# Optimization experiments

Hardware: AMD Instinct MI355X
Metric: run time of the kernel (lower is better)

## Reference

```python
import jax, jax.numpy as jnp
import numpy as np

H, O, M, D, B = 4, 32, 128, 16, 1024
JITTER = 1e-4


def k_rbf(theta, X, Y):
    # theta: [H, 1+D] (log sf2, log lengthscales); X: [O,Mx,D]; Y: [O,My,D]
    sf2 = jnp.exp(theta[:, 0])[:, None, None, None]          # [H,1,1,1]
    ls = jnp.exp(theta[:, 1:])                               # [H,D]
    Xs = X[None] / ls[:, None, None, :]                      # [H,O,Mx,D]
    Ys = Y[None] / ls[:, None, None, :]                      # [H,O,My,D]
    d2 = ((Xs ** 2).sum(-1)[..., :, None]
          + (Ys ** 2).sum(-1)[..., None, :]
          - 2.0 * jnp.einsum('homd,hond->homn', Xs, Ys))
    return sf2 * jnp.exp(-0.5 * jnp.maximum(d2, 0.0))


def vec2tril(vec, m):
    r, c = jnp.tril_indices(m)
    L = jnp.zeros(vec.shape[:-1] + (m, m), vec.dtype)
    return L.at[..., r, c].set(vec)


def _st(Lmat, rhs):
    return jax.scipy.linalg.solve_triangular(Lmat, rhs, lower=True)


def setup_inputs() -> dict:
    key = jax.random.key(0)
    ks = jax.random.split(key, 8)
    eye = jnp.eye(M, dtype=jnp.float32)
    return {
        'x': jax.random.normal(ks[0], (B, D), jnp.float32),
        'z': 0.5 * jax.random.normal(ks[1], (O, M, D), jnp.float32),
        'u_mean': 0.5 * jax.random.normal(ks[2], (O, M, 1), jnp.float32),
        'u_tril_vec': 0.1 * jax.random.normal(ks[3], (O, M * (M + 1) // 2), jnp.float32),
        'm_old': 0.5 * jax.random.normal(ks[4], (O, M, 1), jnp.float32),
        'L_old': jnp.tril(0.1 * jax.random.normal(ks[5], (O, M, M), jnp.float32)) + eye,
        'z_old': 0.5 * jax.random.normal(ks[6], (O, M, D), jnp.float32),
        'theta': 0.1 * jax.random.normal(ks[7], (H, D + 1), jnp.float32),
    }


def reference(x, z, u_mean, u_tril_vec, m_old, L_old, z_old, theta):
    dt = x.dtype
    u_tril = vec2tril(u_tril_vec, M)                          # [O,M,M]
    eyeM = jnp.eye(M, dtype=dt)

    # ---- linear_gauss_joint (one previous task) ----
    kuf = k_rbf(theta, z_old, z)                              # [H,O,M,M]
    kuu = k_rbf(theta, z_old, z_old)                          # [H,O,M,M]
    Lkuu = jnp.linalg.cholesky(kuu + JITTER * eyeM)
    LKinvKuf = _st(Lkuu, kuf)
    m_oldh = jnp.broadcast_to(m_old[None], (H, O, M, 1))
    L_oldh = jnp.broadcast_to(L_old[None], (H, O, M, M))
    LKinvm = _st(Lkuu, m_oldh)
    Am = jnp.einsum('...ij,...ik->...jk', LKinvKuf, LKinvm)   # A @ m_old, [H,O,M,1]
    m_new = Am + u_mean[None]
    m_joint = jnp.concatenate([m_oldh, m_new], axis=-2)       # [H,O,2M,1]

    S_old = jnp.einsum('...ji,...ki->...jk', L_oldh, L_oldh)
    LKinvLS = _st(Lkuu, L_oldh)
    AtX = jnp.einsum('...ij,...ik->...jk', LKinvLS, LKinvKuf)  # [H,O,M,M]
    SoldAt = jnp.einsum('...ji,...ik->...jk', L_oldh, AtX)
    ASoldt = jnp.swapaxes(SoldAt, -1, -2)
    S_cur = jnp.einsum('...ji,...ki->...jk', u_tril, u_tril)[None]
    ASoldAt = jnp.einsum('...ij,...ik->...jk', AtX, AtX)
    cov_joint = jnp.concatenate([
        jnp.concatenate([S_old, SoldAt], axis=-1),
        jnp.concatenate([ASoldt, S_cur + ASoldAt], axis=-1)], axis=-2)
    eye2M = jnp.eye(2 * M, dtype=dt)
    L_joint = jnp.linalg.cholesky(cov_joint + JITTER * eye2M)  # [H,O,2M,2M]
    z_joint = jnp.concatenate([z_old, z], axis=-2)             # [O,2M,D]

    # ---- linear_gauss_conditional_diag ----
    xb = jnp.broadcast_to(x[None], (O, B, D))
    kuf2 = k_rbf(theta, z_joint, xb)                           # [H,O,2M,B]
    kuu2 = k_rbf(theta, z_joint, z_joint)
    Lk2 = jnp.linalg.cholesky(kuu2 + JITTER * eye2M)
    LKinvu = _st(Lk2, m_joint)
    LKinvKuf2 = _st(Lk2, kuf2)
    kff_diag = jnp.exp(theta[:, 0])[:, None, None]             # [H,1,1]
    diag1 = (LKinvKuf2 ** 2).sum(axis=-2)                      # [H,O,B]
    LKinvLs = _st(Lk2, L_joint)
    vec2 = jnp.einsum('...ij,...ik->...jk', LKinvLs, LKinvKuf2)
    diag2 = (vec2 ** 2).sum(axis=-2)
    mu = jnp.einsum('...ij,...ik->...jk', LKinvKuf2, LKinvu)[..., 0]
    var = kff_diag - diag1 + diag2
    return mu, var
```

## Files before the change

kernel.cpp:

```cpp
#include <hip/hip_runtime.h>

#define H_ 4
#define O_ 32
#define HO 128
#define M_ 128
#define M2 256
#define D_ 16
#define B_ 1024
#define JIT 1e-4f

typedef unsigned short ushort_t;
typedef __bf16 v8bf __attribute__((ext_vector_type(8)));
typedef float v16f __attribute__((ext_vector_type(16)));
typedef unsigned short v8us __attribute__((ext_vector_type(8)));
typedef unsigned short v4us __attribute__((ext_vector_type(4)));

__device__ inline void splitbf(float v, ushort_t& hb, ushort_t& lb) {
    unsigned int u = __float_as_uint(v);
    hb = (ushort_t)(u >> 16);
    float hf = __uint_as_float((unsigned int)hb << 16);
    float r = v - hf;
    lb = (ushort_t)(__float_as_uint(r) >> 16);
}
__device__ inline float bf2f(ushort_t u) { return __uint_as_float((unsigned int)u << 16); }

__device__ __forceinline__ float rdlane(float v, int l) {
    return __int_as_float(__builtin_amdgcn_readlane(__float_as_int(v), l));
}

__global__ __launch_bounds__(256) void k_prekuu2(const float* __restrict__ theta,
                                                 const float* __restrict__ x,
                                                 const float* __restrict__ z,
                                                 const float* __restrict__ z_old,
                                                 float* __restrict__ SF2,
                                                 float* __restrict__ XS, float* __restrict__ XN,
                                                 float* __restrict__ ZS, float* __restrict__ ZN,
                                                 float* __restrict__ K2) {
    int bb = blockIdx.x, t = threadIdx.x;
    __shared__ float zs[M2][D_];
    __shared__ float zn[M2];
    __shared__ float ls[D_];
    if (bb == 144) {
        if (t < H_) SF2[t] = __expf(theta[t * (D_ + 1)]);
        return;
    }
    if (bb >= 128) {
        int j = (bb - 128) * 256 + t;
        int h = j >> 10, b = j & 1023;
        if (t < D_) ls[t] = __expf(-theta[h * (D_ + 1) + 1 + t]);
        __syncthreads();
        float s = 0.f;
#pragma unroll
        for (int d = 0; d < D_; d++) {
            float v = x[b * D_ + d] * ls[d];
            XS[(long)j * D_ + d] = v;
            s += v * v;
        }
        XN[j] = s;
        return;
    }
    int pair = bb, h = pair >> 5, o = pair & 31, i = t;
    if (t < D_) ls[t] = __expf(-theta[h * (D_ + 1) + 1 + t]);
    __syncthreads();
    const float* src = (i < M_) ? (z_old + ((long)o * M_ + i) * D_)
                                : (z + ((long)o * M_ + (i - M_)) * D_);
    float s = 0.f;
#pragma unroll
    for (int d = 0; d < D_; d++) {
        float v = src[d] * ls[d];
        zs[i][d] = v;
        ZS[((long)pair * M2 + i) * D_ + d] = v;
        s += v * v;
    }
    zn[i] = s;
    ZN[pair * M2 + i] = s;
    __syncthreads();
    float sf2 = __expf(theta[h * (D_ + 1)]);
    float my[D_];
#pragma unroll
    for (int d = 0; d < D_; d++) my[d] = zs[i][d];
    float myn = zn[i];
    for (int q = 0; q < M2; q++) {
        float dot = 0.f;
#pragma unroll
        for (int d = 0; d < D_; d++) dot += zs[q][d] * my[d];
        float d2 = fmaxf(zn[q] + myn - 2.f * dot, 0.f);
        float v = sf2 * __expf(-0.5f * d2);
        if (q == i) v += JIT;
        K2[(long)pair * M2 * M2 + (long)q * M2 + i] = v;
    }
}

__device__ __forceinline__ void choltri_body(const float* __restrict__ S, int ldsrc,
                                             float* __restrict__ Li, long b1, int t,
                                             float* __restrict__ Ap, float* __restrict__ Lv,
                                             float* __restrict__ Ws4, float* __restrict__ Tm,
                                             float* __restrict__ rdia) {
    for (int e = t; e < M_ * (M_ + 1) / 2; e += 256) {
        int i = (int)((sqrtf(8.f * e + 1.f) - 1.f) * 0.5f);
        while ((i + 1) * (i + 2) / 2 <= e) i++;
        while (i * (i + 1) / 2 > e) i--;
        int j = e - i * (i + 1) / 2;
        Ap[e] = S[(long)i * ldsrc + j];
    }
    __syncthreads();

    int lane = t & 63;
    int wav = t >> 6;
    int r = lane & 31;

    for (int kb = 0; kb < 4; kb++) {
        int c0 = kb * 32;
        if (wav == 0) {
            float a[32];
            int gr = c0 + r;
            int base = gr * (gr + 1) / 2 + c0;
#pragma unroll
            for (int j = 0; j < 32; j++) a[j] = Ap[base + j];
#pragma unroll
            for (int k = 0; k < 32; k++) {
                float dk = rdlane(a[k], k);
                float rs = rsqrtf(dk);
                rs = rs * (1.5f - 0.5f * dk * rs * rs);
                a[k] *= rs;
                if (lane == k) rdia[c0 + k] = rs;
#pragma unroll
                for (int j = k + 1; j < 32; j++) {
                    float ljk = rdlane(a[k], j);
                    a[j] = fmaf(-a[k], ljk, a[j]);
                }
            }
            if (lane < 32) {
#pragma unroll
                for (int j = 0; j < 32; j++)
                    if (j <= r) Ap[base + j] = a[j];
            }
        }
        __syncthreads();
        int R = 96 - c0;
        if (R > 0) {
            if (t < R) {
                int gi = c0 + 32 + t;
                int pb = gi * (gi + 1) / 2 + c0;
                float xr[32];
#pragma unroll
                for (int j = 0; j < 32; j++) xr[j] = Ap[pb + j];
#pragma unroll
                for (int q = 0; q < 32; q++) {
                    float xq = xr[q] * rdia[c0 + q];
                    xr[q] = xq;
#pragma unroll
                    for (int j = q + 1; j < 32; j++)
                        xr[j] = fmaf(-xq, Ap[(c0 + j) * (c0 + j + 1) / 2 + c0 + q], xr[j]);
                }
#pragma unroll
                for (int j = 0; j < 32; j++) Ap[pb + j] = xr[j];
            }
            __syncthreads();
            int nb = R >> 2;
            int ntile = nb * (nb + 1) / 2;
            for (int tp = t; tp < ntile; tp += 256) {
                int bi = (int)((sqrtf(8.f * tp + 1.f) - 1.f) * 0.5f);
                while ((bi + 1) * (bi + 2) / 2 <= tp) bi++;
                while (bi * (bi + 1) / 2 > tp) bi--;
                int bj = tp - bi * (bi + 1) / 2;
                int i0 = c0 + 32 + bi * 4, j0 = c0 + 32 + bj * 4;
                float acc[4][4] = {};
                for (int k = 0; k < 32; k++) {
                    float av[4], bv[4];
#pragma unroll
                    for (int q = 0; q < 4; q++) av[q] = Ap[(i0 + q) * (i0 + q + 1) / 2 + c0 + k];
#pragma unroll
                    for (int rr = 0; rr < 4; rr++) bv[rr] = Ap[(j0 + rr) * (j0 + rr + 1) / 2 + c0 + k];
#pragma unroll
                    for (int q = 0; q < 4; q++)
#pragma unroll
                        for (int rr = 0; rr < 4; rr++) acc[q][rr] += av[q] * bv[rr];
                }
#pragma unroll
                for (int q = 0; q < 4; q++)
#pragma unroll
                    for (int rr = 0; rr < 4; rr++) {
                        int gi = i0 + q, gj = j0 + rr;
                        if (gj <= gi) Ap[gi * (gi + 1) / 2 + gj] -= acc[q][rr];
                    }
            }
            __syncthreads();
        }
    }

    {
        int pb = wav;
        int c0 = pb * 32;
        float a[32];
        int gr = c0 + r;
        int base = gr * (gr + 1) / 2 + c0;
#pragma unroll
        for (int j = 0; j < 32; j++) a[j] = Ap[base + j];
        float wr[32];
#pragma unroll
        for (int i = 0; i < 32; i++) {
            float rdi = rdia[c0 + i];
            float acc = 0.f;
#pragma unroll
            for (int j = 0; j < i; j++) {
                float lij = rdlane(a[j], i);
                acc = fmaf(lij, wr[j], acc);
            }
            wr[i] = (i == r) ? rdi : -acc * rdi;
        }
        if (lane < 32) {
            float* Wp = Ws4 + pb * 1056;
#pragma unroll
            for (int i = 0; i < 32; i++) Wp[i * 33 + r] = wr[i];
        }
    }
    __syncthreads();

    for (int e = t; e < 16384; e += 256) {
        int i = e >> 7, j = e & 127;
        int bi = i >> 5, bj = j >> 5;
        float v = 0.f;
        if (bi == bj) v = Ws4[bi * 1056 + (i & 31) * 33 + (j & 31)];
        Lv[i * 132 + j] = v;
    }
    __syncthreads();
    for (int d = 1; d < 4; d++) {
        int nblk = 4 - d;
        int ne = nblk * 256;
        for (int p = t; p < ne; p += 256) {
            int b = p >> 8, rc = p & 255;
            int rr = rc >> 3, c4 = (rc & 7) * 4;
            int ib = b + d;
            int grow = ib * 32 + rr;
            int abase = grow * (grow + 1) / 2;
            float a0 = 0.f, a1 = 0.f, a2 = 0.f, a3 = 0.f;
            for (int k = b; k < ib; k++) {
                const float* Arow = Ap + abase + k * 32;
                const float* L0 = Lv + (k * 32) * 132 + b * 32 + c4;
#pragma unroll
                for (int q = 0; q < 32; q++) {
                    float av = Arow[q];
                    const float* Lr = L0 + q * 132;
                    a0 = fmaf(av, Lr[0], a0);
                    a1 = fmaf(av, Lr[1], a1);
                    a2 = fmaf(av, Lr[2], a2);
                    a3 = fmaf(av, Lr[3], a3);
                }
            }
            float* Tp = Tm + b * 1152 + rr * 36 + c4;
            Tp[0] = a0; Tp[1] = a1; Tp[2] = a2; Tp[3] = a3;
        }
        __syncthreads();
        for (int p = t; p < ne; p += 256) {
            int b = p >> 8, rc = p & 255;
            int rr = rc >> 3, c4 = (rc & 7) * 4;
            int ib = b + d;
            const float* Wp = Ws4 + ib * 1056 + rr * 33;
            const float* T0 = Tm + b * 1152 + c4;
            float a0 = 0.f, a1 = 0.f, a2 = 0.f, a3 = 0.f;
#pragma unroll
            for (int q = 0; q < 32; q++) {
                float wq = Wp[q];
                const float* Tq = T0 + q * 36;
                a0 = fmaf(wq, Tq[0], a0);
                a1 = fmaf(wq, Tq[1], a1);
                a2 = fmaf(wq, Tq[2], a2);
                a3 = fmaf(wq, Tq[3], a3);
            }
            float* Op = Lv + (ib * 32 + rr) * 132 + b * 32 + c4;
            Op[0] = -a0; Op[1] = -a1; Op[2] = -a2; Op[3] = -a3;
        }
        __syncthreads();
    }
    for (int e = t; e < 16384; e += 256) {
        int i = e >> 7, j = e & 127;
        Li[b1 + e] = Lv[i * 132 + j];
    }
}

#define SH_TOTAL (8256 + 16896 + 4224 + 3456 + 128)

__global__ __launch_bounds__(256) void k_choltri_tl(const float* __restrict__ src,
                                                    float* __restrict__ Li,
                                                    const float* __restrict__ L_old,
                                                    const float* __restrict__ vec,
                                                    ushort_t* __restrict__ WTh,
                                                    ushort_t* __restrict__ WTl) {
    int bb = blockIdx.x, t = threadIdx.x;
    __shared__ __align__(16) float SH[SH_TOTAL];
    if (bb < 128) {
        choltri_body(src + (long)bb * ((long)M2 * M2), M2, Li, (long)bb * 16384, t,
                     SH, SH + 8256, SH + 8256 + 16896, SH + 8256 + 16896 + 4224,
                     SH + 8256 + 16896 + 4224 + 3456);
        return;
    }
    int pair = bb - 128, o = pair & 31;
    long b2 = (long)pair * 65536;
    float* vs = SH;
    float(*tile)[33] = (float(*)[33])(SH + 8256);
    for (int e = t; e < M_ * (M_ + 1) / 2; e += 256) vs[e] = vec[(long)o * (M_ * (M_ + 1) / 2) + e];
    __syncthreads();
    for (int e = t; e < 16384; e += 256) {
        int n = e >> 7, k = e & 127;
        float v = (k >= n) ? vs[k * (k + 1) / 2 + n] : 0.f;
        ushort_t hb, lb;
        splitbf(v, hb, lb);
        long a = b2 + (long)(128 + n) * 256 + 128 + k;
        WTh[a] = hb;
        WTl[a] = lb;
    }
    for (int e = t; e < 16384; e += 256) {
        int n = e >> 7, k = e & 127;
        long a = b2 + (long)(128 + n) * 256 + k;
        WTh[a] = 0;
        WTl[a] = 0;
    }
    const float* sp = L_old + (long)o * 16384;
    int tx = t & 31, ty = t >> 5;
    for (int bi = 0; bi < 4; bi++)
        for (int bj = 0; bj < 4; bj++) {
            __syncthreads();
            for (int r = ty; r < 32; r += 8)
                tile[r][tx] = sp[(long)(bi * 32 + r) * 128 + bj * 32 + tx];
            __syncthreads();
            for (int r = ty; r < 32; r += 8) {
                ushort_t hb, lb;
                splitbf(tile[tx][r], hb, lb);
                long a = b2 + (long)(bj * 32 + r) * 256 + bi * 32 + tx;
                WTh[a] = hb;
                WTl[a] = lb;
            }
        }
}

__global__ __launch_bounds__(256) void k_choltri_br(const float* __restrict__ src,
                                                    float* __restrict__ Li,
                                                    const float* __restrict__ A1,
                                                    const float* __restrict__ Linv1,
                                                    float* __restrict__ T1g,
                                                    const float* __restrict__ BLW,
                                                    ushort_t* __restrict__ LTh,
                                                    ushort_t* __restrict__ LTl,
                                                    ushort_t* __restrict__ WTh,
                                                    ushort_t* __restrict__ WTl) {
    int bb = blockIdx.x, t = threadIdx.x;
    __shared__ __align__(16) float SH[SH_TOTAL];
    if (bb < 128) {
        choltri_body(src + (long)bb * ((long)M2 * M2), M2, Li, (long)bb * 16384, t,
                     SH, SH + 8256, SH + 8256 + 16896, SH + 8256 + 16896 + 4224,
                     SH + 8256 + 16896 + 4224 + 3456);
        return;
    }
    if (bb < 256) {
        int pair = bb - 128;
        long b1 = (long)pair * 16384;
        float(*As)[132] = (float(*)[132])(SH + 8256);
        float(*Bs)[132] = ((float(*)[132])(SH + 8256)) + 16;
        const float* Apt = A1 + b1;
        const float* Bpt = Linv1 + b1;
        float* Cp = T1g + (long)pair * 65536;
        int tx = t & 15, ty = t >> 4;
        float acc[8][8] = {};
        for (int kt = 0; kt < M_; kt += 16) {
#pragma unroll
            for (int q = 0; q < 8; q++) {
                int e = q * 256 + t;
                int kk = e >> 7, m = e & 127;
                As[kk][m] = Apt[(long)(kt + kk) * 128 + m];
                Bs[kk][m] = Bpt[(long)(kt + kk) * 128 + m];
            }
            __syncthreads();
#pragma unroll
            for (int kk = 0; kk < 16; kk++) {
                float a[8], b[8];
#pragma unroll
                for (int q = 0; q < 8; q++) { a[q] = As[kk][ty + 16 * q]; b[q] = Bs[kk][tx + 16 * q]; }
#pragma unroll
                for (int q = 0; q < 8; q++)
#pragma unroll
                    for (int r = 0; r < 8; r++) acc[q][r] += a[q] * b[r];
            }
            __syncthreads();
        }
#pragma unroll
        for (int q = 0; q < 8; q++)
#pragma unroll
            for (int r = 0; r < 8; r++)
                Cp[(long)(ty + 16 * q) * 128 + tx + 16 * r] = acc[q][r];
        return;
    }
    if (bb < 384) {
        int pair = bb - 256;
        long b2 = (long)pair * 65536, b1 = (long)pair * 16384;
        float(*tile)[33] = (float(*)[33])(SH + 8256);
        for (int e = t; e < 16384; e += 256) {
            int n = e >> 7, k = e & 127;
            long a = b2 + (long)(128 + n) * 256 + k;
            LTh[a] = 0;
            LTl[a] = 0;
        }
        const float* sp = Linv1 + b1;
        int tx = t & 31, ty = t >> 5;
        for (int bi = 0; bi < 4; bi++)
            for (int bj = 0; bj < 4; bj++) {
                __syncthreads();
                for (int r = ty; r < 32; r += 8)
                    tile[r][tx] = sp[(long)(bi * 32 + r) * 128 + bj * 32 + tx];
                __syncthreads();
                for (int r = ty; r < 32; r += 8) {
                    ushort_t hb, lb;
                    splitbf(tile[tx][r], hb, lb);
                    long a = b2 + (long)(bj * 32 + r) * 256 + bi * 32 + tx;
                    LTh[a] = hb;
                    LTl[a] = lb;
                }
            }
        return;
    }
    {
        int pair = bb - 384;
        long b2 = (long)pair * 65536, b1 = (long)pair * 16384;
        float(*tile)[33] = (float(*)[33])(SH + 8256);
        const float* sp = BLW + b1;
        int tx = t & 31, ty = t >> 5;
        for (int bi = 0; bi < 4; bi++)
            for (int bj = 0; bj < 4; bj++) {
                __syncthreads();
                for (int r = ty; r < 32; r += 8)
                    tile[r][tx] = sp[(long)(bi * 32 + r) * 128 + bj * 32 + tx];
                __syncthreads();
                for (int r = ty; r < 32; r += 8) {
                    ushort_t hb, lb;
                    splitbf(tile[tx][r], hb, lb);
                    long a = b2 + (long)(bj * 32 + r) * 256 + 128 + bi * 32 + tx;
                    WTh[a] = hb;
                    WTl[a] = lb;
                }
            }
    }
}

__global__ __launch_bounds__(256) void k_a1a3(const float* __restrict__ Linv1,
                                              const float* __restrict__ KUU2,
                                              const float* __restrict__ L_old,
                                              float* __restrict__ A1, float* __restrict__ A3) {
    int pair = blockIdx.x, y = blockIdx.y, o = pair & 31;
    const float* Ap = Linv1 + (long)pair * 16384;
    const float* Bp = y ? (L_old + (long)o * 16384) : (KUU2 + (long)pair * 65536 + 128);
    int ldb = y ? 128 : 256;
    float* Cp = (y ? A3 : A1) + (long)pair * 16384;
    int t = threadIdx.x, tx = t & 15, ty = t >> 4;
    __shared__ float As[16][132], Bs[16][132];
    float acc[8][8] = {};
    for (int kt = 0; kt < M_; kt += 16) {
#pragma unroll
        for (int q = 0; q < 8; q++) {
            int e = q * 256 + t;
            int m = e >> 4, kk = e & 15;
            As[kk][m] = Ap[(long)m * 128 + kt + kk];
            int kk2 = e >> 7, n = e & 127;
            Bs[kk2][n] = Bp[(long)(kt + kk2) * ldb + n];
        }
        __syncthreads();
#pragma unroll
        for (int kk = 0; kk < 16; kk++) {
            float a[8], b[8];
#pragma unroll
            for (int q = 0; q < 8; q++) { a[q] = As[kk][ty + 16 * q]; b[q] = Bs[kk][tx + 16 * q]; }
#pragma unroll
            for (int q = 0; q < 8; q++)
#pragma unroll
                for (int r = 0; r < 8; r++) acc[q][r] += a[q] * b[r];
        }
        __syncthreads();
    }
#pragma unroll
    for (int q = 0; q < 8; q++)
#pragma unroll
        for (int r = 0; r < 8; r++)
            Cp[(long)(ty + 16 * q) * 128 + tx + 16 * r] = acc[q][r];
}

__global__ __launch_bounds__(256) void k_blwschur(const float* __restrict__ A1,
                                                  const float* __restrict__ A3,
                                                  float* __restrict__ BLW,
                                                  float* __restrict__ KUU2,
                                                  const float* __restrict__ Linv1,
                                                  const float* __restrict__ m_old,
                                                  const float* __restrict__ u_mean,
                                                  float* __restrict__ MJ,
                                                  float* __restrict__ CV) {
    int pair = blockIdx.x, y = blockIdx.y, o = pair & 31;
    int t = threadIdx.x;
    if (y == 2) {
        CV[pair * 256 + t] = 0.f;
        __shared__ float mo[128], a2[128];
        if (t < 128) mo[t] = m_old[o * 128 + t];
        __syncthreads();
        if (t < 128) {
            const float* Lr = Linv1 + (long)pair * 16384 + (long)t * 128;
            float acc = 0.f;
            for (int j = 0; j <= t; j++) acc += Lr[j] * mo[j];
            a2[t] = acc;
        }
        __syncthreads();
        if (t < 128) {
            float m = 0.f;
            for (int i = 0; i < 128; i++) m += A1[(long)pair * 16384 + (long)i * 128 + t] * a2[i];
            MJ[pair * 256 + t] = mo[t];
            MJ[pair * 256 + 128 + t] = m + u_mean[o * 128 + t];
        }
        return;
    }
    const float* Ap = A1 + (long)pair * 16384;
    const float* Bp = (y ? A1 : A3) + (long)pair * 16384;
    float* Cp;
    int ldc;
    if (y) { Cp = KUU2 + (long)pair * 65536 + 128L * 256 + 128; ldc = 256; }
    else   { Cp = BLW + (long)pair * 16384; ldc = 128; }
    int tx = t & 15, ty = t >> 4;
    __shared__ float As[16][132], Bs[16][132];
    float acc[8][8] = {};
    for (int kt = 0; kt < M_; kt += 16) {
#pragma unroll
        for (int q = 0; q < 8; q++) {
            int e = q * 256 + t;
            int kk = e >> 7, m = e & 127;
            As[kk][m] = Ap[(long)(kt + kk) * 128 + m];
            Bs[kk][m] = Bp[(long)(kt + kk) * 128 + m];
        }
        __syncthreads();
#pragma unroll
        for (int kk = 0; kk < 16; kk++) {
            float a[8], b[8];
#pragma unroll
            for (int q = 0; q < 8; q++) { a[q] = As[kk][ty + 16 * q]; b[q] = Bs[kk][tx + 16 * q]; }
#pragma unroll
            for (int q = 0; q < 8; q++)
#pragma unroll
                for (int r = 0; r < 8; r++) acc[q][r] += a[q] * b[r];
        }
        __syncthreads();
    }
#pragma unroll
    for (int q = 0; q < 8; q++)
#pragma unroll
        for (int r = 0; r < 8; r++) {
            long idx = (long)(ty + 16 * q) * ldc + tx + 16 * r;
            if (y) Cp[idx] -= acc[q][r];
            else Cp[idx] = acc[q][r];
        }
}

__global__ __launch_bounds__(256) void k_blicalc2(const float* __restrict__ Linv2,
                                                  const float* __restrict__ T1g,
                                                  ushort_t* __restrict__ LTh,
                                                  ushort_t* __restrict__ LTl) {
    int pair = blockIdx.x, t = threadIdx.x, tx = t & 15, ty = t >> 4;
    long b1 = (long)pair * 16384, b2 = (long)pair * 65536;
    __shared__ float T1s[128][129];
    __shared__ float As[16][132], Bs[16][132];
    const float* Apt = Linv2 + b1;
    const float* Bpt = T1g + (long)pair * 65536;
    float acc[8][8] = {};
    for (int kt = 0; kt < M_; kt += 16) {
#pragma unroll
        for (int q = 0; q < 8; q++) {
            int e = q * 256 + t;
            int m = e >> 4, kk = e & 15;
            As[kk][m] = Apt[(long)m * 128 + kt + kk];
            int kk2 = e >> 7, n = e & 127;
            Bs[kk2][n] = Bpt[(long)(kt + kk2) * 128 + n];
        }
        __syncthreads();
#pragma unroll
        for (int kk = 0; kk < 16; kk++) {
            float a[8], b[8];
#pragma unroll
            for (int q = 0; q < 8; q++) { a[q] = As[kk][ty + 16 * q]; b[q] = Bs[kk][tx + 16 * q]; }
#pragma unroll
            for (int q = 0; q < 8; q++)
#pragma unroll
                for (int r = 0; r < 8; r++) acc[q][r] += a[q] * b[r];
        }
        __syncthreads();
    }
#pragma unroll
    for (int q = 0; q < 8; q++)
#pragma unroll
        for (int r = 0; r < 8; r++) T1s[ty + 16 * q][tx + 16 * r] = -acc[q][r];
    __syncthreads();
    for (int e = t; e < 16384; e += 256) {
        int j = e >> 7, i = e & 127;
        ushort_t hb, lb;
        splitbf(T1s[i][j], hb, lb);
        long a = b2 + (long)j * 256 + 128 + i;
        LTh[a] = hb;
        LTl[a] = lb;
    }
    __syncthreads();
    for (int e = t; e < 16384; e += 256) {
        int i = e >> 7, j = e & 127;
        T1s[i][j] = Apt[(long)i * 128 + j];
    }
    __syncthreads();
    for (int e = t; e < 16384; e += 256) {
        int n = e >> 7, k = e & 127;
        ushort_t hb, lb;
        splitbf(T1s[k][n], hb, lb);
        long a = b2 + (long)(128 + n) * 256 + 128 + k;
        LTh[a] = hb;
        LTl[a] = lb;
    }
}

#define BSTR 56
template <int TILES3>
__global__ __launch_bounds__(256) void k_bmmx(const ushort_t* __restrict__ Ah,
                                              const ushort_t* __restrict__ Al,
                                              const ushort_t* __restrict__ Bh,
                                              const ushort_t* __restrict__ Bl,
                                              float* __restrict__ Cf,
                                              ushort_t* __restrict__ Chi,
                                              ushort_t* __restrict__ Clo,
                                              const float* __restrict__ Dm,
                                              int kLoMode, float alpha,
                                              const float* __restrict__ MJv,
                                              float* __restrict__ CVat) {
    int pair = blockIdx.x;
    long base = (long)pair * 65536;
    int I0, J0, mir = 0;
    if (TILES3) {
        int qb = blockIdx.y;
        I0 = (qb == 0) ? 0 : 128;
        J0 = (qb == 2) ? 0 : I0;
        mir = (qb == 2);
    } else {
        I0 = (blockIdx.y >> 1) * 128;
        J0 = (blockIdx.y & 1) * 128;
    }
    int k0 = (kLoMode == 1) ? max(I0, J0) : (kLoMode == 2) ? J0 : 0;
    int t = threadIdx.x;
    int w = t >> 6, lane = t & 63;
    int l31 = lane & 31, lhalf = lane >> 5;
    int wy = w >> 1, wx = w & 1;

    __shared__ __align__(16) ushort_t AsH[128][BSTR], AsL[128][BSTR];
    __shared__ __align__(16) ushort_t BsH[128][BSTR], BsL[128][BSTR];

    v16f acc[2][2];
#pragma unroll
    for (int mt = 0; mt < 2; mt++)
#pragma unroll
        for (int nt = 0; nt < 2; nt++)
#pragma unroll
            for (int r = 0; r < 16; r++) acc[mt][nt][r] = 0.f;

    for (int kt = k0; kt < 256; kt += 32) {
        __syncthreads();
#pragma unroll
        for (int u = 0; u < 2; u++) {
            int idx = u * 256 + t;
            int m = idx >> 2, kc = (idx & 3) * 8;
            long arow = base + (long)(I0 + m) * 256 + kt + kc;
            long brow = base + (long)(J0 + m) * 256 + kt + kc;
            *(v8us*)&AsH[m][kc] = *(const v8us*)(Ah + arow);
            *(v8us*)&AsL[m][kc] = *(const v8us*)(Al + arow);
            *(v8us*)&BsH[m][kc] = *(const v8us*)(Bh + brow);
            *(v8us*)&BsL[m][kc] = *(const v8us*)(Bl + brow);
        }
        __syncthreads();
#pragma unroll
        for (int ks = 0; ks < 2; ks++) {
            int ko = ks * 16 + lhalf * 8;
            v8bf ah[2], al[2], bh[2], bl[2];
#pragma unroll
            for (int mt = 0; mt < 2; mt++) {
                int r = wy * 64 + mt * 32 + l31;
                ah[mt] = *(const v8bf*)&AsH[r][ko];
                al[mt] = *(const v8bf*)&AsL[r][ko];
            }
#pragma unroll
            for (int nt = 0; nt < 2; nt++) {
                int r = wx * 64 + nt * 32 + l31;
                bh[nt] = *(const v8bf*)&BsH[r][ko];
                bl[nt] = *(const v8bf*)&BsL[r][ko];
            }
#pragma unroll
            for (int mt = 0; mt < 2; mt++)
#pragma unroll
                for (int nt = 0; nt < 2; nt++) {
                    acc[mt][nt] = __builtin_amdgcn_mfma_f32_32x32x16_bf16(ah[mt], bh[nt], acc[mt][nt], 0, 0, 0);
                    acc[mt][nt] = __builtin_amdgcn_mfma_f32_32x32x16_bf16(ah[mt], bl[nt], acc[mt][nt], 0, 0, 0);
                    acc[mt][nt] = __builtin_amdgcn_mfma_f32_32x32x16_bf16(al[mt], bh[nt], acc[mt][nt], 0, 0, 0);
                }
        }
    }

    float mjc[2] = {0.f, 0.f};
    float cvmir[2] = {0.f, 0.f};
    if (MJv) {
#pragma unroll
        for (int nt = 0; nt < 2; nt++)
            mjc[nt] = MJv[(long)pair * 256 + J0 + wx * 64 + nt * 32 + l31];
    }
#pragma unroll
    for (int mt = 0; mt < 2; mt++) {
#pragma unroll
        for (int r = 0; r < 16; r++) {
            int row = I0 + wy * 64 + mt * 32 + 8 * (r >> 2) + 4 * lhalf + (r & 3);
            float rowsum = 0.f;
            float mjrow = 0.f;
            if (MJv && mir) mjrow = MJv[(long)pair * 256 + row];
#pragma unroll
            for (int nt = 0; nt < 2; nt++) {
                int col = J0 + wx * 64 + nt * 32 + l31;
                long idx = base + (long)row * 256 + col;
                float v = alpha * acc[mt][nt][r];
                if (Dm) v += Dm[idx];
                ushort_t hb, lb;
                splitbf(v, hb, lb);
                if (Cf) Cf[idx] = v;
                if (Chi) { Chi[idx] = hb; Clo[idx] = lb; }
                if (mir) {
                    long idxT = base + (long)col * 256 + row;
                    if (Cf) Cf[idxT] = v;
                    if (Chi) { Chi[idxT] = hb; Clo[idxT] = lb; }
                }
                if (MJv) {
                    rowsum += v * mjc[nt];
                    if (mir) cvmir[nt] += v * mjrow;
                }
            }
            if (MJv) {
#pragma unroll
                for (int m = 1; m < 32; m <<= 1) rowsum += __shfl_xor(rowsum, m, 64);
                if (l31 == 0) atomicAdd(&CVat[(long)pair * 256 + row], rowsum);
            }
        }
    }
    if (MJv && mir) {
#pragma unroll
        for (int nt = 0; nt < 2; nt++)
            atomicAdd(&CVat[(long)pair * 256 + J0 + wx * 64 + nt * 32 + l31], cvmir[nt]);
    }
}

#define KTP 280
__global__ __launch_bounds__(256) void k_kbuild(const float* __restrict__ ZS, const float* __restrict__ ZN,
                                                const float* __restrict__ XS, const float* __restrict__ XN,
                                                const float* __restrict__ SF2, const float* __restrict__ CV,
                                                ushort_t* __restrict__ Kg, float* __restrict__ out) {
    int bt = blockIdx.x;
    int pair = blockIdx.y;
    int h = pair >> 5;
    int t = threadIdx.x;
    int w = t >> 6;
    int b = t & 63;

    __shared__ __align__(16) ushort_t KbT[64][KTP];
    __shared__ float mup[4][64];

    float sf2 = SF2[h];
    long bg = (long)h * B_ + bt * 64 + b;
    const float4* xrow = (const float4*)(XS + bg * 16);
    float4 x0 = xrow[0], x1 = xrow[1], x2 = xrow[2], x3 = xrow[3];
    float xn = XN[bg];
    float mupart = 0.f;
    const float* cvp = CV + pair * 256;
    const float* znp = ZN + pair * 256;
#pragma unroll 2
    for (int j8 = 0; j8 < 8; j8++) {
        v8us kb8;
#pragma unroll
        for (int e = 0; e < 8; e++) {
            int j = w * 64 + j8 * 8 + e;
            const float4* zrow = (const float4*)(ZS + ((long)pair * 256 + j) * 16);
            float4 z0 = zrow[0], z1 = zrow[1], z2 = zrow[2], z3 = zrow[3];
            float dot = z0.x * x0.x + z0.y * x0.y + z0.z * x0.z + z0.w * x0.w +
                        z1.x * x1.x + z1.y * x1.y + z1.z * x1.z + z1.w * x1.w +
                        z2.x * x2.x + z2.y * x2.y + z2.z * x2.z + z2.w * x2.w +
                        z3.x * x3.x + z3.y * x3.y + z3.z * x3.z + z3.w * x3.w;
            float d2 = fmaxf(znp[j] + xn - 2.f * dot, 0.f);
            float kv = sf2 * __expf(-0.5f * d2);
            mupart += cvp[j] * kv;
            unsigned int u = __float_as_uint(kv);
            u += 0x7fffu + ((u >> 16) & 1u);
            kb8[e] = (unsigned short)(u >> 16);
        }
        *(v8us*)&KbT[b][w * 64 + j8 * 8] = kb8;
    }
    mup[w][b] = mupart;
    __syncthreads();
    long kbase = ((long)pair * 1024 + bt * 64) * 256;
#pragma unroll
    for (int e = 0; e < 8; e++) {
        int c = e * 256 + t;
        int bb = c >> 5, cj = (c & 31) * 8;
        *(v8us*)(Kg + kbase + (long)bb * 256 + cj) = *(const v8us*)&KbT[bb][cj];
    }
    if (t < 64) {
        float mu = mup[0][t] + mup[1][t] + mup[2][t] + mup[3][t];
        out[(long)pair * 1024 + bt * 64 + t] = mu;
    }
}

#define KT2 264
__global__ __launch_bounds__(256) void k_kb4(const ushort_t* __restrict__ Kg,
                                             const ushort_t* __restrict__ Ghi,
                                             const ushort_t* __restrict__ Glo,
                                             const float* __restrict__ SF2, float* __restrict__ out) {
    int pair = blockIdx.x & 127;
    int bt = blockIdx.x >> 7;
    int h = pair >> 5;
    int t = threadIdx.x;
    int w = t >> 6;
    int lane = t & 63;
    int l31 = lane & 31, lhalf = lane >> 5;

    __shared__ __align__(16) ushort_t KbT[128][KT2];
    __shared__ float qpart[4][128];

    float sf2 = SF2[h];
    long kbase = ((long)pair * 1024 + bt * 128) * 256;
#pragma unroll
    for (int e = 0; e < 16; e++) {
        int c = e * 256 + t;
        int bb = c >> 5, cj = (c & 31) * 8;
        *(v8us*)&KbT[bb][cj] = *(const v8us*)(Kg + kbase + (long)bb * 256 + cj);
    }
    __syncthreads();

    v16f acc[2][4];
#pragma unroll
    for (int mt = 0; mt < 2; mt++)
#pragma unroll
        for (int nt = 0; nt < 4; nt++)
#pragma unroll
            for (int r = 0; r < 16; r++) acc[mt][nt][r] = 0.f;

    const ushort_t* GhiP = Ghi + (long)pair * 65536;
    const ushort_t* GloP = Glo + (long)pair * 65536;
#pragma unroll 2
    for (int k0 = 0; k0 < 256; k0 += 16) {
        v8bf bfr[4];
#pragma unroll
        for (int nt = 0; nt < 4; nt++)
            bfr[nt] = *(const v8bf*)&KbT[nt * 32 + l31][k0 + lhalf * 8];
#pragma unroll
        for (int mt = 0; mt < 2; mt++) {
            int i = w * 64 + mt * 32 + l31;
            v8bf ah = *(const v8bf*)(GhiP + (long)i * 256 + k0 + lhalf * 8);
            v8bf al = *(const v8bf*)(GloP + (long)i * 256 + k0 + lhalf * 8);
#pragma unroll
            for (int nt = 0; nt < 4; nt++) {
                acc[mt][nt] = __builtin_amdgcn_mfma_f32_32x32x16_bf16(ah, bfr[nt], acc[mt][nt], 0, 0, 0);
                acc[mt][nt] = __builtin_amdgcn_mfma_f32_32x32x16_bf16(al, bfr[nt], acc[mt][nt], 0, 0, 0);
            }
        }
    }

    float qp[4] = {0.f, 0.f, 0.f, 0.f};
#pragma unroll
    for (int mt = 0; mt < 2; mt++) {
#pragma unroll
        for (int nt = 0; nt < 4; nt++) {
            int b = nt * 32 + l31;
#pragma unroll
            for (int g = 0; g < 4; g++) {
                int ibase = w * 64 + mt * 32 + 8 * g + 4 * lhalf;
                v4us k4 = *(const v4us*)&KbT[b][ibase];
#pragma unroll
                for (int e = 0; e < 4; e++) {
                    float kv = bf2f(k4[e]);
                    qp[nt] += kv * acc[mt][nt][4 * g + e];
                }
            }
        }
    }
#pragma unroll
    for (int nt = 0; nt < 4; nt++) {
        qp[nt] += __shfl_down(qp[nt], 32, 64);
        if (lhalf == 0) qpart[w][nt * 32 + l31] = qp[nt];
    }
    __syncthreads();

    if (t < 128) {
        float q = qpart[0][t] + qpart[1][t] + qpart[2][t] + qpart[3][t];
        out[(long)H_ * O_ * B_ + (long)pair * 1024 + bt * 128 + t] = sf2 - q;
    }
}

extern "C" void kernel_launch(void* const* d_in, const int* in_sizes, int n_in,
                              void* d_out, int out_size, void* d_ws, size_t ws_size,
                              hipStream_t stream) {
    const float* x = (const float*)d_in[0];
    const float* z = (const float*)d_in[1];
    const float* u_mean = (const float*)d_in[2];
    const float* u_tril_vec = (const float*)d_in[3];
    const float* m_old = (const float*)d_in[4];
    const float* L_old = (const float*)d_in[5];
    const float* z_old = (const float*)d_in[6];
    const float* theta = (const float*)d_in[7];

    const long BIGSZ = (long)HO * M2 * M2;
    const long MSZ = (long)HO * M_ * M_;

    float* ws = (float*)d_ws;
    long off = 0;
    float* BIG0 = ws + off; off += BIGSZ;
    float* BIG1 = ws + off; off += BIGSZ;
    float* BIG2 = ws + off; off += BIGSZ;
    float* BIG3 = ws + off; off += BIGSZ;
    float* ZS = ws + off; off += (long)HO * M2 * D_;
    float* XS = ws + off; off += (long)H_ * B_ * D_;
    float* ZN = ws + off; off += (long)HO * M2;
    float* XN = ws + off; off += (long)H_ * B_;
    float* MJ = ws + off; off += (long)HO * M2;
    float* CV = ws + off; off += (long)HO * M2;
    float* SF2v = ws + off; off += H_;

    float* KUU2 = BIG0;
    float* AINV = BIG0;
    float* T1g = BIG0;
    float* Linv1 = BIG2;
    float* A1 = BIG2 + MSZ;
    float* A3 = BIG2 + 2 * MSZ;
    float* Linv2 = BIG2 + 2 * MSZ;
    float* BLW = BIG2 + 3 * MSZ;
    ushort_t* LINVTh = (ushort_t*)BIG1;
    ushort_t* LINVTl = LINVTh + BIGSZ;
    ushort_t* AINVh = (ushort_t*)BIG2;
    ushort_t* AINVl = AINVh + BIGSZ;
    ushort_t* WcTh = (ushort_t*)BIG3;
    ushort_t* WcTl = WcTh + BIGSZ;
    ushort_t* Yh = (ushort_t*)BIG1;
    ushort_t* Yl = Yh + BIGSZ;
    ushort_t* Ghi = (ushort_t*)BIG3;
    ushort_t* Glo = Ghi + BIGSZ;
    ushort_t* Kg = (ushort_t*)BIG1;
    const long BRoff = 128L * M2 + 128;

    k_prekuu2<<<145, 256, 0, stream>>>(theta, x, z, z_old, SF2v, XS, XN, ZS, ZN, KUU2);
    k_choltri_tl<<<256, 256, 0, stream>>>(KUU2, Linv1, L_old, u_tril_vec, WcTh, WcTl);
    k_a1a3<<<dim3(HO, 2), 256, 0, stream>>>(Linv1, KUU2, L_old, A1, A3);
    k_blwschur<<<dim3(HO, 3), 256, 0, stream>>>(A1, A3, BLW, KUU2, Linv1, m_old, u_mean, MJ, CV);
    k_choltri_br<<<512, 256, 0, stream>>>(KUU2 + BRoff, Linv2, A1, Linv1, T1g, BLW,
                                          LINVTh, LINVTl, WcTh, WcTl);
    k_blicalc2<<<HO, 256, 0, stream>>>(Linv2, T1g, LINVTh, LINVTl);
    k_bmmx<1><<<dim3(HO, 3), 256, 0, stream>>>(LINVTh, LINVTl, LINVTh, LINVTl,
                                               AINV, AINVh, AINVl, nullptr, 1, 1.f, MJ, CV);
    k_bmmx<0><<<dim3(HO, 4), 256, 0, stream>>>(AINVh, AINVl, WcTh, WcTl,
                                               nullptr, Yh, Yl, nullptr, 2, 1.f, nullptr, nullptr);
    k_bmmx<1><<<dim3(HO, 3), 256, 0, stream>>>(Yh, Yl, Yh, Yl,
                                               nullptr, Ghi, Glo, AINV, 0, -1.f, nullptr, nullptr);
    k_kbuild<<<dim3(16, HO), 256, 0, stream>>>(ZS, ZN, XS, XN, SF2v, CV, Kg, (float*)d_out);
    k_kb4<<<1024, 256, 0, stream>>>(Kg, Ghi, Glo, SF2v, (float*)d_out);
}
```

Baseline: 611.2 us.

## Pad packed triangular LDS layout for float4 access and split kuu2 build

Replaces the plain packed-triangular shared-memory layout in the Cholesky/triangular-inverse body with a padded layout whose rows are 16-byte aligned. The global load, the trailing-update inner products and the block-inverse multiplies can then use float4 LDS reads and writes. The W and T scratch tiles get a stride of 36 to keep float4 alignment. Separately, the kuu2 build splits each (h,o) pair across two blocks, one per half of the rows, which doubles the grid for more parallelism at the cost of redundant z scaling. The trade-offs are more shared memory use and changed bank-conflict patterns.

```diff
diff --git a/kernel.cpp b/kernel.cpp
--- a/kernel.cpp
+++ b/kernel.cpp
@@ -26,6 +26,11 @@
 
 __device__ __forceinline__ float rdlane(float v, int l) {
     return __int_as_float(__builtin_amdgcn_readlane(__float_as_int(v), l));
+}
+
+__device__ __forceinline__ int ro_(int i) {
+    int M = i >> 2, k = i & 3;
+    return 4 * (M + 1) * (2 * M + k);
 }
 
 __global__ __launch_bounds__(256) void k_prekuu2(const float* __restrict__ theta,
@@ -40,12 +45,12 @@
     __shared__ float zs[M2][D_];
     __shared__ float zn[M2];
     __shared__ float ls[D_];
-    if (bb == 144) {
+    if (bb == 272) {
         if (t < H_) SF2[t] = __expf(theta[t * (D_ + 1)]);
         return;
     }
-    if (bb >= 128) {
-        int j = (bb - 128) * 256 + t;
+    if (bb >= 256) {
+        int j = (bb - 256) * 256 + t;
         int h = j >> 10, b = j & 1023;
         if (t < D_) ls[t] = __expf(-theta[h * (D_ + 1) + 1 + t]);
         __syncthreads();
@@ -59,7 +64,8 @@
         XN[j] = s;
         return;
     }
-    int pair = bb, h = pair >> 5, o = pair & 31, i = t;
+    int pair = bb >> 1, half = bb & 1;
+    int h = pair >> 5, o = pair & 31, i = t;
     if (t < D_) ls[t] = __expf(-theta[h * (D_ + 1) + 1 + t]);
     __syncthreads();
     const float* src = (i < M_) ? (z_old + ((long)o * M_ + i) * D_)
@@ -69,18 +75,19 @@
     for (int d = 0; d < D_; d++) {
         float v = src[d] * ls[d];
         zs[i][d] = v;
-        ZS[((long)pair * M2 + i) * D_ + d] = v;
+        if (half == 0) ZS[((long)pair * M2 + i) * D_ + d] = v;
         s += v * v;
     }
     zn[i] = s;
-    ZN[pair * M2 + i] = s;
+    if (half == 0) ZN[pair * M2 + i] = s;
     __syncthreads();
     float sf2 = __expf(theta[h * (D_ + 1)]);
     float my[D_];
 #pragma unroll
     for (int d = 0; d < D_; d++) my[d] = zs[i][d];
     float myn = zn[i];
-    for (int q = 0; q < M2; q++) {
+    int q0 = half * 128;
+    for (int q = q0; q < q0 + 128; q++) {
         float dot = 0.f;
 #pragma unroll
         for (int d = 0; d < D_; d++) dot += zs[q][d] * my[d];
@@ -91,17 +98,30 @@
     }
 }
 
+#define AP_SZ 8448
+#define LV_SZ 16896
+#define WS_SZ 4608
+#define TM_SZ 3456
+#define SH_TOTAL (AP_SZ + LV_SZ + WS_SZ + TM_SZ + 128)
+
 __device__ __forceinline__ void choltri_body(const float* __restrict__ S, int ldsrc,
                                              float* __restrict__ Li, long b1, int t,
                                              float* __restrict__ Ap, float* __restrict__ Lv,
                                              float* __restrict__ Ws4, float* __restrict__ Tm,
                                              float* __restrict__ rdia) {
-    for (int e = t; e < M_ * (M_ + 1) / 2; e += 256) {
-        int i = (int)((sqrtf(8.f * e + 1.f) - 1.f) * 0.5f);
-        while ((i + 1) * (i + 2) / 2 <= e) i++;
-        while (i * (i + 1) / 2 > e) i--;
-        int j = e - i * (i + 1) / 2;
-        Ap[e] = S[(long)i * ldsrc + j];
+#pragma unroll
+    for (int u = 0; u < 16; u++) {
+        int idx = u * 256 + t;
+        int i = idx >> 5, jc = (idx & 31) * 4;
+        float4 v = *(const float4*)(S + (long)i * ldsrc + jc);
+        int tb = ro_(i) + jc;
+        if (jc + 3 <= i) {
+            *(float4*)&Ap[tb] = v;
+        } else if (jc <= i) {
+            Ap[tb] = v.x;
+            if (jc + 1 <= i) Ap[tb + 1] = v.y;
+            if (jc + 2 <= i) Ap[tb + 2] = v.z;
+        }
     }
     __syncthreads();
 
@@ -114,7 +134,7 @@
         if (wav == 0) {
             float a[32];
             int gr = c0 + r;
-            int base = gr * (gr + 1) / 2 + c0;
+            int base = ro_(gr) + c0;
 #pragma unroll
             for (int j = 0; j < 32; j++) a[j] = Ap[base + j];
 #pragma unroll
@@ -141,7 +161,7 @@
         if (R > 0) {
             if (t < R) {
                 int gi = c0 + 32 + t;
-                int pb = gi * (gi + 1) / 2 + c0;
+                int pb = ro_(gi) + c0;
                 float xr[32];
 #pragma unroll
                 for (int j = 0; j < 32; j++) xr[j] = Ap[pb + j];
@@ -151,7 +171,7 @@
                     xr[q] = xq;
 #pragma unroll
                     for (int j = q + 1; j < 32; j++)
-                        xr[j] = fmaf(-xq, Ap[(c0 + j) * (c0 + j + 1) / 2 + c0 + q], xr[j]);
+                        xr[j] = fmaf(-xq, Ap[ro_(c0 + j) + c0 + q], xr[j]);
                 }
 #pragma unroll
                 for (int j = 0; j < 32; j++) Ap[pb + j] = xr[j];
@@ -165,24 +185,34 @@
                 while (bi * (bi + 1) / 2 > tp) bi--;
                 int bj = tp - bi * (bi + 1) / 2;
                 int i0 = c0 + 32 + bi * 4, j0 = c0 + 32 + bj * 4;
+                int ra[4], rb[4];
+#pragma unroll
+                for (int q = 0; q < 4; q++) {
+                    ra[q] = ro_(i0 + q) + c0;
+                    rb[q] = ro_(j0 + q) + c0;
+                }
                 float acc[4][4] = {};
-                for (int k = 0; k < 32; k++) {
-                    float av[4], bv[4];
-#pragma unroll
-                    for (int q = 0; q < 4; q++) av[q] = Ap[(i0 + q) * (i0 + q + 1) / 2 + c0 + k];
-#pragma unroll
-                    for (int rr = 0; rr < 4; rr++) bv[rr] = Ap[(j0 + rr) * (j0 + rr + 1) / 2 + c0 + k];
+#pragma unroll
+                for (int k4 = 0; k4 < 8; k4++) {
+                    float4 av[4], bv[4];
+#pragma unroll
+                    for (int q = 0; q < 4; q++) {
+                        av[q] = *(const float4*)&Ap[ra[q] + k4 * 4];
+                        bv[q] = *(const float4*)&Ap[rb[q] + k4 * 4];
+                    }
 #pragma unroll
                     for (int q = 0; q < 4; q++)
 #pragma unroll
-                        for (int rr = 0; rr < 4; rr++) acc[q][rr] += av[q] * bv[rr];
+                        for (int rr = 0; rr < 4; rr++)
+                            acc[q][rr] += av[q].x * bv[rr].x + av[q].y * bv[rr].y +
+                                          av[q].z * bv[rr].z + av[q].w * bv[rr].w;
                 }
 #pragma unroll
                 for (int q = 0; q < 4; q++)
 #pragma unroll
                     for (int rr = 0; rr < 4; rr++) {
                         int gi = i0 + q, gj = j0 + rr;
-                        if (gj <= gi) Ap[gi * (gi + 1) / 2 + gj] -= acc[q][rr];
+                        if (gj <= gi) Ap[ro_(gi) + gj] -= acc[q][rr];
                     }
             }
             __syncthreads();
@@ -194,7 +224,7 @@
         int c0 = pb * 32;
         float a[32];
         int gr = c0 + r;
-        int base = gr * (gr + 1) / 2 + c0;
+        int base = ro_(gr) + c0;
 #pragma unroll
         for (int j = 0; j < 32; j++) a[j] = Ap[base + j];
         float wr[32];
@@ -210,19 +240,19 @@
             wr[i] = (i == r) ? rdi : -acc * rdi;
         }
         if (lane < 32) {
-            float* Wp = Ws4 + pb * 1056;
-#pragma unroll
-            for (int i = 0; i < 32; i++) Wp[i * 33 + r] = wr[i];
-        }
-    }
-    __syncthreads();
-
-    for (int e = t; e < 16384; e += 256) {
-        int i = e >> 7, j = e & 127;
+            float* Wp = Ws4 + pb * 1152;
+#pragma unroll
+            for (int i = 0; i < 32; i++) Wp[i * 36 + r] = wr[i];
+        }
+    }
+    __syncthreads();
+
+    for (int e = t; e < 4096; e += 256) {
+        int i = e >> 5, j = (e & 31) * 4;
         int bi = i >> 5, bj = j >> 5;
-        float v = 0.f;
-        if (bi == bj) v = Ws4[bi * 1056 + (i & 31) * 33 + (j & 31)];
-        Lv[i * 132 + j] = v;
+        float4 v = make_float4(0.f, 0.f, 0.f, 0.f);
+        if (bi == bj) v = *(const float4*)&Ws4[bi * 1152 + (i & 31) * 36 + (j & 31)];
+        *(float4*)&Lv[i * 132 + j] = v;
     }
     __syncthreads();
     for (int d = 1; d < 4; d++) {
@@ -232,54 +262,60 @@
             int b = p >> 8, rc = p & 255;
             int rr = rc >> 3, c4 = (rc & 7) * 4;
             int ib = b + d;
-            int grow = ib * 32 + rr;
-            int abase = grow * (grow + 1) / 2;
-            float a0 = 0.f, a1 = 0.f, a2 = 0.f, a3 = 0.f;
+            int abase = ro_(ib * 32 + rr);
+            float4 acc = make_float4(0.f, 0.f, 0.f, 0.f);
             for (int k = b; k < ib; k++) {
                 const float* Arow = Ap + abase + k * 32;
                 const float* L0 = Lv + (k * 32) * 132 + b * 32 + c4;
 #pragma unroll
-                for (int q = 0; q < 32; q++) {
-                    float av = Arow[q];
-                    const float* Lr = L0 + q * 132;
-                    a0 = fmaf(av, Lr[0], a0);
-                    a1 = fmaf(av, Lr[1], a1);
-                    a2 = fmaf(av, Lr[2], a2);
-                    a3 = fmaf(av, Lr[3], a3);
-                }
-            }
-            float* Tp = Tm + b * 1152 + rr * 36 + c4;
-            Tp[0] = a0; Tp[1] = a1; Tp[2] = a2; Tp[3] = a3;
+                for (int q4 = 0; q4 < 8; q4++) {
+                    float4 ar = *(const float4*)(Arow + q4 * 4);
+                    const float* Lq = L0 + (q4 * 4) * 132;
+                    float4 l0 = *(const float4*)(Lq);
+                    float4 l1 = *(const float4*)(Lq + 132);
+                    float4 l2 = *(const float4*)(Lq + 264);
+                    float4 l3 = *(const float4*)(Lq + 396);
+                    acc.x += ar.x * l0.x + ar.y * l1.x + ar.z * l2.x + ar.w * l3.x;
+                    acc.y += ar.x * l0.y + ar.y * l1.y + ar.z * l2.y + ar.w * l3.y;
+                    acc.z += ar.x * l0.z + ar.y * l1.z + ar.z * l2.z + ar.w * l3.z;
+                    acc.w += ar.x * l0.w + ar.y * l1.w + ar.z * l2.w + ar.w * l3.w;
+                }
+            }
+            *(float4*)(Tm + b * 1152 + rr * 36 + c4) = acc;
         }
         __syncthreads();
         for (int p = t; p < ne; p += 256) {
             int b = p >> 8, rc = p & 255;
             int rr = rc >> 3, c4 = (rc & 7) * 4;
             int ib = b + d;
-            const float* Wp = Ws4 + ib * 1056 + rr * 33;
+            const float* Wp = Ws4 + ib * 1152 + rr * 36;
             const float* T0 = Tm + b * 1152 + c4;
-            float a0 = 0.f, a1 = 0.f, a2 = 0.f, a3 = 0.f;
-#pragma unroll
-            for (int q = 0; q < 32; q++) {
-                float wq = Wp[q];
-                const float* Tq = T0 + q * 36;
-                a0 = fmaf(wq, Tq[0], a0);
-                a1 = fmaf(wq, Tq[1], a1);
-                a2 = fmaf(wq, Tq[2], a2);
-                a3 = fmaf(wq, Tq[3], a3);
-            }
-            float* Op = Lv + (ib * 32 + rr) * 132 + b * 32 + c4;
-            Op[0] = -a0; Op[1] = -a1; Op[2] = -a2; Op[3] = -a3;
-        }
-        __syncthreads();
-    }
-    for (int e = t; e < 16384; e += 256) {
-        int i = e >> 7, j = e & 127;
-        Li[b1 + e] = Lv[i * 132 + j];
-    }
-}
-
-#define SH_TOTAL (8256 + 16896 + 4224 + 3456 + 128)
+            float4 acc = make_float4(0.f, 0.f, 0.f, 0.f);
+#pragma unroll
+            for (int q4 = 0; q4 < 8; q4++) {
+                float4 w4 = *(const float4*)(Wp + q4 * 4);
+                const float* Tq = T0 + (q4 * 4) * 36;
+                float4 t0 = *(const float4*)(Tq);
+                float4 t1 = *(const float4*)(Tq + 36);
+                float4 t2 = *(const float4*)(Tq + 72);
+                float4 t3 = *(const float4*)(Tq + 108);
+                acc.x += w4.x * t0.x + w4.y * t1.x + w4.z * t2.x + w4.w * t3.x;
+                acc.y += w4.x * t0.y + w4.y * t1.y + w4.z * t2.y + w4.w * t3.y;
+                acc.z += w4.x * t0.z + w4.y * t1.z + w4.z * t2.z + w4.w * t3.z;
+                acc.w += w4.x * t0.w + w4.y * t1.w + w4.z * t2.w + w4.w * t3.w;
+            }
+            *(float4*)(Lv + (ib * 32 + rr) * 132 + b * 32 + c4) =
+                make_float4(-acc.x, -acc.y, -acc.z, -acc.w);
+        }
+        __syncthreads();
+    }
+#pragma unroll
+    for (int u = 0; u < 16; u++) {
+        int idx = u * 256 + t;
+        int i = idx >> 5, jc = (idx & 31) * 4;
+        *(float4*)(Li + b1 + (long)i * 128 + jc) = *(const float4*)(Lv + i * 132 + jc);
+    }
+}
 
 __global__ __launch_bounds__(256) void k_choltri_tl(const float* __restrict__ src,
                                                     float* __restrict__ Li,
@@ -291,14 +327,14 @@
     __shared__ __align__(16) float SH[SH_TOTAL];
     if (bb < 128) {
         choltri_body(src + (long)bb * ((long)M2 * M2), M2, Li, (long)bb * 16384, t,
-                     SH, SH + 8256, SH + 8256 + 16896, SH + 8256 + 16896 + 4224,
-                     SH + 8256 + 16896 + 4224 + 3456);
+                     SH, SH + AP_SZ, SH + AP_SZ + LV_SZ, SH + AP_SZ + LV_SZ + WS_SZ,
+                     SH + AP_SZ + LV_SZ + WS_SZ + TM_SZ);
         return;
     }
     int pair = bb - 128, o = pair & 31;
     long b2 = (long)pair * 65536;
     float* vs = SH;
-    float(*tile)[33] = (float(*)[33])(SH + 8256);
+    float(*tile)[33] = (float(*)[33])(SH + AP_SZ);
     for (int e = t; e < M_ * (M_ + 1) / 2; e += 256) vs[e] = vec[(long)o * (M_ * (M_ + 1) / 2) + e];
     __syncthreads();
     for (int e = t; e < 16384; e += 256) {
@@ -348,15 +384,15 @@
     __shared__ __align__(16) float SH[SH_TOTAL];
     if (bb < 128) {
         choltri_body(src + (long)bb * ((long)M2 * M2), M2, Li, (long)bb * 16384, t,
-                     SH, SH + 8256, SH + 8256 + 16896, SH + 8256 + 16896 + 4224,
-                     SH + 8256 + 16896 + 4224 + 3456);
+                     SH, SH + AP_SZ, SH + AP_SZ + LV_SZ, SH + AP_SZ + LV_SZ + WS_SZ,
+                     SH + AP_SZ + LV_SZ + WS_SZ + TM_SZ);
         return;
     }
     if (bb < 256) {
         int pair = bb - 128;
         long b1 = (long)pair * 16384;
-        float(*As)[132] = (float(*)[132])(SH + 8256);
-        float(*Bs)[132] = ((float(*)[132])(SH + 8256)) + 16;
+        float(*As)[132] = (float(*)[132])(SH + AP_SZ);
+        float(*Bs)[132] = ((float(*)[132])(SH + AP_SZ)) + 16;
         const float* Apt = A1 + b1;
         const float* Bpt = Linv1 + b1;
         float* Cp = T1g + (long)pair * 65536;
@@ -393,7 +429,7 @@
     if (bb < 384) {
         int pair = bb - 256;
         long b2 = (long)pair * 65536, b1 = (long)pair * 16384;
-        float(*tile)[33] = (float(*)[33])(SH + 8256);
+        float(*tile)[33] = (float(*)[33])(SH + AP_SZ);
         for (int e = t; e < 16384; e += 256) {
             int n = e >> 7, k = e & 127;
             long a = b2 + (long)(128 + n) * 256 + k;
@@ -421,7 +457,7 @@
     {
         int pair = bb - 384;
         long b2 = (long)pair * 65536, b1 = (long)pair * 16384;
-        float(*tile)[33] = (float(*)[33])(SH + 8256);
+        float(*tile)[33] = (float(*)[33])(SH + AP_SZ);
         const float* sp = BLW + b1;
         int tx = t & 31, ty = t >> 5;
         for (int bi = 0; bi < 4; bi++)
@@ -942,7 +978,7 @@
     ushort_t* Kg = (ushort_t*)BIG1;
     const long BRoff = 128L * M2 + 128;
 
-    k_prekuu2<<<145, 256, 0, stream>>>(theta, x, z, z_old, SF2v, XS, XN, ZS, ZN, KUU2);
+    k_prekuu2<<<273, 256, 0, stream>>>(theta, x, z, z_old, SF2v, XS, XN, ZS, ZN, KUU2);
     k_choltri_tl<<<256, 256, 0, stream>>>(KUU2, Linv1, L_old, u_tril_vec, WcTh, WcTl);
     k_a1a3<<<dim3(HO, 2), 256, 0, stream>>>(Linv1, KUU2, L_old, A1, A3);
     k_blwschur<<<dim3(HO, 3), 256, 0, stream>>>(A1, A3, BLW, KUU2, Linv1, m_old, u_mean, MJ, CV);
```

Result: faster. 576.6 us (-5.7%).
